# Optimization experiments

Hardware: AMD Instinct MI355X
Metric: run time of the kernel (lower is better)

Reference implementation:

```python
import jax, jax.numpy as jnp
import numpy as np

N0, N1 = 81, 319          # hard-coded split t1[:, :81] / t1[:, 81:]
C_OUT = 64
LAYERS = 5
EPS = 1e-5


def _temporal_conv(X, w1, b1, wc, bc):
    # X: [B, N, T, Cin] -> NCHW with H=N, W=T, kernel (1, 3), VALID
    out_ch = w1.shape[0]
    Xp = jnp.transpose(X, (0, 3, 1, 2))
    dn = ('NCHW', 'OIHW', 'NCHW')
    conv = lambda x, w: jax.lax.conv_general_dilated(x, w, (1, 1), 'VALID', dimension_numbers=dn)
    xc = conv(Xp, wc) + bc[None, :, None, None]
    temp = conv(Xp, w1) + b1[None, :, None, None]
    x_p, x_q = xc[:, :out_ch], xc[:, out_ch:]
    out = (x_p + temp) * jax.nn.sigmoid(x_q)
    return jnp.transpose(out, (0, 2, 3, 1))  # [B, N, T-2, out_ch]


def _het_conv(X0l, X1l, X00, Aaa, Aab, Aba, th1, th2, th3):
    # torch einsum('ij,jklm->kilm', A, X.permute(1,0,2,3)) == einsum('ij,bjtc->bitc', A, X)
    u1 = jnp.einsum('ij,bjtc->bitc', Aaa, X0l)
    u2 = jax.nn.relu(u1 @ th1)
    u3 = jnp.einsum('ij,bjtc->bitc', Aab @ Aba, X0l)
    u4 = jnp.einsum('ij,bjtc->bitc', Aab, X1l)
    u5 = jax.nn.sigmoid(u3 @ th2 + u4 @ th3)
    u6 = jax.nn.relu((u2 + u5) * 0.5)
    return jax.nn.relu(0.9 * u6 + 0.1 * X00)


def setup_inputs() -> dict:
    key = jax.random.key(0)
    ks = jax.random.split(key, 24)
    B, N, T, Cin = 16, 400, 32, 2
    stdv = 1.0 / np.sqrt(C_OUT)
    u = lambda k, shape, s: jax.random.uniform(k, shape, jnp.float32, -s, s)
    inp = {
        'X': jax.random.normal(ks[0], (B, N, T, Cin), jnp.float32),
        'A00': jax.random.uniform(ks[1], (N0, N0), jnp.float32) / N0,
        'A01': jax.random.uniform(ks[2], (N0, N1), jnp.float32) / N1,
        'A10': jax.random.uniform(ks[3], (N1, N0), jnp.float32) / N0,
        'A11': jax.random.uniform(ks[4], (N1, N1), jnp.float32) / N1,
        't1_conv1_w': jax.random.normal(ks[5], (C_OUT, Cin, 1, 3), jnp.float32) * 0.1,
        't1_conv1_b': jnp.zeros((C_OUT,), jnp.float32),
        't1_causal_w': jax.random.normal(ks[6], (2 * C_OUT, Cin, 1, 3), jnp.float32) * 0.1,
        't1_causal_b': jnp.zeros((2 * C_OUT,), jnp.float32),
        'g1_th1': u(ks[7], (LAYERS, C_OUT, C_OUT), stdv),
        'g1_th2': u(ks[8], (LAYERS, C_OUT, C_OUT), stdv),
        'g1_th3': u(ks[9], (LAYERS, C_OUT, C_OUT), stdv),
        'g2_th1': u(ks[10], (LAYERS, C_OUT, C_OUT), stdv),
        'g2_th2': u(ks[11], (LAYERS, C_OUT, C_OUT), stdv),
        'g2_th3': u(ks[12], (LAYERS, C_OUT, C_OUT), stdv),
        'theta': u(ks[13], (C_OUT, C_OUT), stdv),
        't2_conv1_w': jax.random.normal(ks[14], (C_OUT, C_OUT, 1, 3), jnp.float32) * 0.05,
        't2_conv1_b': jnp.zeros((C_OUT,), jnp.float32),
        't2_causal_w': jax.random.normal(ks[15], (2 * C_OUT, C_OUT, 1, 3), jnp.float32) * 0.05,
        't2_causal_b': jnp.zeros((2 * C_OUT,), jnp.float32),
        'bn_gamma': jnp.ones((N,), jnp.float32),
        'bn_beta': jnp.zeros((N,), jnp.float32),
    }
    return inp


def reference(X, A00, A01, A10, A11, t1_conv1_w, t1_conv1_b, t1_causal_w, t1_causal_b,
              g1_th1, g1_th2, g1_th3, g2_th1, g2_th2, g2_th3, theta,
              t2_conv1_w, t2_conv1_b, t2_causal_w, t2_causal_b, bn_gamma, bn_beta):
    t1 = _temporal_conv(X, t1_conv1_w, t1_conv1_b, t1_causal_w, t1_causal_b)  # [B,N,T-2,64]
    X0, X1 = t1[:, :N0], t1[:, N0:]
    u0, u1v = X0, X1
    for i in range(LAYERS):
        u0 = _het_conv(u0, u1v, X0, A00, A01, A10, g1_th1[i], g1_th2[i], g1_th3[i])
        u1v = _het_conv(u1v, u0, X1, A11, A10, A01, g2_th1[i], g2_th2[i], g2_th3[i])
    tk = jnp.concatenate([u0, u1v], axis=1)            # [B,N,T-2,64]
    tk = jax.nn.relu(tk @ theta)
    tk = _temporal_conv(tk, t2_conv1_w, t2_conv1_b, t2_causal_w, t2_causal_b)  # [B,N,T-4,64]
    # BatchNorm2d(num_nodes): channel axis is the node axis (dim 1), training-mode batch stats
    mean = tk.mean(axis=(0, 2, 3), keepdims=True)
    var = tk.var(axis=(0, 2, 3), keepdims=True)
    return (tk - mean) / jnp.sqrt(var + EPS) * bn_gamma[None, :, None, None] + bn_beta[None, :, None, None]
```

## Files before the change

### kernel.cpp

```cpp
#include <hip/hip_runtime.h>


typedef __attribute__((ext_vector_type(8))) short short8v;
typedef __attribute__((ext_vector_type(4))) short short4v;
typedef __attribute__((ext_vector_type(4))) float f32x4;

#define BB 16
#define NA 81
#define NB 319
#define PA 128
#define PB 320
#define M1 1920
#define T1 30
#define T2 28

#define MFMA16 __builtin_amdgcn_mfma_f32_16x16x32_bf16

__device__ __forceinline__ float sigmoidf_(float x){ return 1.0f/(1.0f+__expf(-x)); }
__device__ __forceinline__ short f2bf(float f){
  unsigned u = __float_as_uint(f);
  u += 0x7FFF + ((u>>16)&1);
  return (short)(u>>16);
}
__device__ __forceinline__ float bf2f(short s){
  return __uint_as_float(((unsigned)(unsigned short)s)<<16);
}

__global__ __launch_bounds__(256) void k_prep_mm(const float* __restrict__ A01,
                                                 const float* __restrict__ A10,
                                                 float* __restrict__ Ma) {
  int idx = blockIdx.x*256 + threadIdx.x;
  if (idx >= NA*NA) return;
  int i = idx / NA, j = idx % NA;
  float a = 0.f;
  for (int k = 0; k < NB; ++k) a += A01[i*NB + k]*A10[k*NA + j];
  Ma[idx] = a;
}

__device__ __forceinline__ void packA_one(int f, const float* src, int I, int J,
                                          int ld, int nIt, short* dst) {
  int e = f & 7, l = (f >> 3) & 63, rest = f >> 9;
  int it = rest % nIt, jt = rest / nIt;
  int i = it*16 + (l & 15);
  int j = jt*32 + (l >> 4)*8 + e;
  float v = (i < I && j < J) ? src[i*ld + j] : 0.f;
  dst[f] = f2bf(v);
}

__global__ __launch_bounds__(256) void k_pack_A(
    const float* __restrict__ A00, const float* __restrict__ A01,
    const float* __restrict__ A10, const float* __restrict__ A11,
    const float* __restrict__ Ma,
    short* __restrict__ A00pk, short* __restrict__ Mapk,
    short* __restrict__ A01pk, short* __restrict__ A10pk,
    short* __restrict__ A11pk) {
  int idx = blockIdx.x*256 + threadIdx.x;
  if (idx < 12288)        { packA_one(idx, A00, NA, NA, NA, 8,  A00pk); return; }
  idx -= 12288;
  if (idx < 12288)        { packA_one(idx, Ma,  NA, NA, NA, 8,  Mapk);  return; }
  idx -= 12288;
  if (idx < 40960)        { packA_one(idx, A01, NA, NB, NB, 8,  A01pk); return; }
  idx -= 40960;
  if (idx < 30720)        { packA_one(idx, A10, NB, NA, NA, 20, A10pk); return; }
  idx -= 30720;
  if (idx < 102400)       { packA_one(idx, A11, NB, NB, NB, 20, A11pk); return; }
}

__global__ __launch_bounds__(256) void k_pack_th(
    const float* __restrict__ g1t1, const float* __restrict__ g1t2,
    const float* __restrict__ g1t3, const float* __restrict__ g2t1,
    const float* __restrict__ g2t2, const float* __restrict__ g2t3,
    const float* __restrict__ theta,
    const float* __restrict__ w12, const float* __restrict__ wc2,
    const float* __restrict__ w11, const float* __restrict__ wc1,
    const float* __restrict__ b11, const float* __restrict__ bc1,
    short* __restrict__ thpk, short* __restrict__ thetapk,
    short* __restrict__ W2pk, float* __restrict__ W1t, float* __restrict__ B1t) {
  int idx = blockIdx.x*256 + threadIdx.x;
  if (idx < 122880) {
    int mat = idx / 4096, rem = idx % 4096;
    int ct = rem / 1024, ks = (rem / 512) & 1, l = (rem >> 3) & 63, e = rem & 7;
    int ci = ks*32 + (l >> 4)*8 + e, co = ct*16 + (l & 15);
    int layer = mat / 6, which = mat % 6;
    const float* src = which == 0 ? g1t1 : which == 1 ? g1t2 : which == 2 ? g1t3
                     : which == 3 ? g2t1 : which == 4 ? g2t2 : g2t3;
    thpk[idx] = f2bf(src[layer*4096 + ci*64 + co]);
    return;
  }
  idx -= 122880;
  if (idx < 4096) {
    int ct = idx / 1024, ks = (idx / 512) & 1, l = (idx >> 3) & 63, e = idx & 7;
    int ci = ks*32 + (l >> 4)*8 + e, co = ct*16 + (l & 15);
    thetapk[idx] = f2bf(theta[ci*64 + co]);
    return;
  }
  idx -= 4096;
  if (idx < 36864) {
    int ct = idx / 3072, rem = idx % 3072;
    int ks = rem / 512, l = (rem >> 3) & 63, e = rem & 7;
    int kap = ks*32 + (l >> 4)*8 + e;
    int k = kap >> 6, ci = kap & 63;
    int cc = ct*16 + (l & 15);
    float v = (cc < 64) ? w12[cc*192 + ci*3 + k] : wc2[(cc - 64)*192 + ci*3 + k];
    W2pk[idx] = f2bf(v);
    return;
  }
  idx -= 36864;
  if (idx < 1152) {
    int kk = idx / 192, cc = idx % 192;
    int k = kk >> 1, ci = kk & 1;
    W1t[idx] = (cc < 64) ? w11[cc*6 + ci*3 + k] : wc1[(cc - 64)*6 + ci*3 + k];
    return;
  }
  idx -= 1152;
  if (idx < 192) { B1t[idx] = (idx < 64) ? b11[idx] : bc1[idx - 64]; return; }
}

__global__ __launch_bounds__(192) void k_tconv1(const float* __restrict__ X,
                                                const float* __restrict__ W1t,
                                                const float* __restrict__ B1t,
                                                short* __restrict__ t1a,
                                                short* __restrict__ t1b) {
  __shared__ float xl[64];
  __shared__ float wl[6*192];
  __shared__ float bl[192];
  __shared__ float ol[T1*192];
  int bn = blockIdx.x;
  int b = bn / 400, n = bn % 400;
  int tid = threadIdx.x;
  if (tid < 64) xl[tid] = X[(size_t)bn*64 + tid];
  for (int i2 = tid; i2 < 6*192; i2 += 192) wl[i2] = W1t[i2];
  bl[tid] = B1t[tid];
  __syncthreads();
  float acc[T1];
  float bias = bl[tid];
#pragma unroll
  for (int t = 0; t < T1; ++t) acc[t] = bias;
#pragma unroll
  for (int kk = 0; kk < 6; ++kk) {
    float w = wl[kk*192 + tid];
    int k = kk >> 1, ci = kk & 1;
#pragma unroll
    for (int t = 0; t < T1; ++t) acc[t] += xl[(t + k)*2 + ci]*w;
  }
#pragma unroll
  for (int t = 0; t < T1; ++t) ol[t*192 + tid] = acc[t];
  __syncthreads();
  short* dst = (n < NA) ? (t1a + ((size_t)b*PA + n)*M1)
                        : (t1b + ((size_t)b*PB + (n - NA))*M1);
  for (int p = tid; p < T1*64; p += 192) {
    int t = p >> 6, c = p & 63;
    float v = (ol[t*192 + 64 + c] + ol[t*192 + c])*sigmoidf_(ol[t*192 + 128 + c]);
    dst[p] = f2bf(v);
  }
}

__global__ __launch_bounds__(256) void k_transpose(const short* __restrict__ src,
                                                   short* __restrict__ dst, int Ipad) {
  int lane = threadIdx.x & 63, wv = threadIdx.x >> 6;
  int n = blockIdx.x*64 + lane;
  int b = blockIdx.z;
  const short* sp = src + ((size_t)b*Ipad + n)*M1;
  int mbase = (blockIdx.y*4 + wv)*120;
  for (int k = 0; k < 120; k += 8) {
    int m = mbase + k;
    short8v v = *(const short8v*)(sp + m);
#pragma unroll
    for (int e = 0; e < 8; ++e)
      dst[((size_t)b*M1 + m + e)*Ipad + n] = v[e];
  }
}

template<int KT12, int KT3>
__global__ __launch_bounds__(64, 1) void k_layer_a(
    const short* __restrict__ XT12, int Jp12,
    const short* __restrict__ XT3, int Jp3,
    const short* __restrict__ Apk1, const short* __restrict__ Apk2, int nIt12,
    const short* __restrict__ Apk3, int nIt3,
    const short* __restrict__ th1, const short* __restrict__ th2,
    const short* __restrict__ th3,
    const short* __restrict__ X00, short* __restrict__ uout,
    short* __restrict__ umT, short* __restrict__ g3T,
    int NW, int I, int IpadO) {
  __shared__ short sd[3][32*68];
  int lane = threadIdx.x & 63;
  int ln = lane & 15, qw = lane >> 4;

  int total = NW*30*BB;
  int d = blockIdx.x;
  int logical = (d & 7)*(total >> 3) + (d >> 3);
  int w = logical % NW;
  int rest = logical / NW;
  int mt = rest % 30;
  int b = rest / 30;

  int m0 = mt*64;
  int t = mt;

  short* s1 = sd[0];
  short* s2 = sd[1];
  short* s3 = sd[2];

  short8v x0r[4];
#pragma unroll
  for (int kq = 0; kq < 4; ++kq) {
    int il = kq*8 + (lane >> 3);
    int irow = w*32 + il;
    if (irow >= I) irow = I - 1;
    size_t ro = ((size_t)b*IpadO + irow)*M1 + t*64 + (lane & 7)*8;
    x0r[kq] = *(const short8v*)(X00 + ro);
  }

  {
    f32x4 a3[2][4];
#pragma unroll
    for (int ft = 0; ft < 2; ++ft)
#pragma unroll
      for (int mf = 0; mf < 4; ++mf) a3[ft][mf] = (f32x4)0.f;

    short8v xa[2][4];
    short8v b3f[2][2];
#pragma unroll
    for (int mf = 0; mf < 4; ++mf) {
      size_t ro = ((size_t)b*M1 + m0 + mf*16 + ln)*Jp3 + qw*8;
      xa[0][mf] = *(const short8v*)(XT3 + ro);
    }
    {
      size_t ab = (((size_t)0*nIt3 + w*2)*64 + lane)*8;
      b3f[0][0] = *(const short8v*)(Apk3 + ab);
      b3f[0][1] = *(const short8v*)(Apk3 + ab + 512);
    }
#pragma unroll
    for (int ks = 0; ks < KT3; ++ks) {
      if (ks + 1 < KT3) {
        int nx = (ks + 1) & 1;
#pragma unroll
        for (int mf = 0; mf < 4; ++mf) {
          size_t ro = ((size_t)b*M1 + m0 + mf*16 + ln)*Jp3 + (ks + 1)*32 + qw*8;
          xa[nx][mf] = *(const short8v*)(XT3 + ro);
        }
        size_t ab = (((size_t)(ks + 1)*nIt3 + w*2)*64 + lane)*8;
        b3f[nx][0] = *(const short8v*)(Apk3 + ab);
        b3f[nx][1] = *(const short8v*)(Apk3 + ab + 512);
      }
      int cu = ks & 1;
#pragma unroll
      for (int mf = 0; mf < 4; ++mf) {
        a3[0][mf] = MFMA16(xa[cu][mf], b3f[cu][0], a3[0][mf], 0, 0, 0);
        a3[1][mf] = MFMA16(xa[cu][mf], b3f[cu][1], a3[1][mf], 0, 0, 0);
      }
    }
#pragma unroll
    for (int ft = 0; ft < 2; ++ft)
#pragma unroll
      for (int mf = 0; mf < 4; ++mf) {
        int irow = ft*16 + ln;
        int cc = mf*16 + qw*4;
        short4v v3;
#pragma unroll
        for (int r = 0; r < 4; ++r) v3[r] = f2bf(a3[ft][mf][r]);
        *(short4v*)(s3 + irow*68 + cc) = v3;
      }
  }
  {
    int co = lane;
    size_t cb = ((size_t)b*M1 + t*64 + co)*IpadO + w*32;
#pragma unroll
    for (int kq = 0; kq < 4; ++kq) {
      short8v v;
#pragma unroll
      for (int ii = 0; ii < 8; ++ii) v[ii] = s3[(kq*8 + ii)*68 + co];
      *(short8v*)(g3T + cb + kq*8) = v;
    }
  }

  {
    f32x4 a1[2][4], a2[2][4];
#pragma unroll
    for (int ft = 0; ft < 2; ++ft)
#pragma unroll
      for (int mf = 0; mf < 4; ++mf) { a1[ft][mf] = (f32x4)0.f; a2[ft][mf] = (f32x4)0.f; }

    short8v xa[2][4];
    short8v b1f[2][2], b2f[2][2];
#pragma unroll
    for (int mf = 0; mf < 4; ++mf) {
      size_t ro = ((size_t)b*M1 + m0 + mf*16 + ln)*Jp12 + qw*8;
      xa[0][mf] = *(const short8v*)(XT12 + ro);
    }
    {
      size_t ab = (((size_t)0*nIt12 + w*2)*64 + lane)*8;
      b1f[0][0] = *(const short8v*)(Apk1 + ab);
      b1f[0][1] = *(const short8v*)(Apk1 + ab + 512);
      b2f[0][0] = *(const short8v*)(Apk2 + ab);
      b2f[0][1] = *(const short8v*)(Apk2 + ab + 512);
    }
#pragma unroll
    for (int ks = 0; ks < KT12; ++ks) {
      if (ks + 1 < KT12) {
        int nx = (ks + 1) & 1;
#pragma unroll
        for (int mf = 0; mf < 4; ++mf) {
          size_t ro = ((size_t)b*M1 + m0 + mf*16 + ln)*Jp12 + (ks + 1)*32 + qw*8;
          xa[nx][mf] = *(const short8v*)(XT12 + ro);
        }
        size_t ab = (((size_t)(ks + 1)*nIt12 + w*2)*64 + lane)*8;
        b1f[nx][0] = *(const short8v*)(Apk1 + ab);
        b1f[nx][1] = *(const short8v*)(Apk1 + ab + 512);
        b2f[nx][0] = *(const short8v*)(Apk2 + ab);
        b2f[nx][1] = *(const short8v*)(Apk2 + ab + 512);
      }
      int cu = ks & 1;
#pragma unroll
      for (int mf = 0; mf < 4; ++mf) {
        a1[0][mf] = MFMA16(xa[cu][mf], b1f[cu][0], a1[0][mf], 0, 0, 0);
        a1[1][mf] = MFMA16(xa[cu][mf], b1f[cu][1], a1[1][mf], 0, 0, 0);
        a2[0][mf] = MFMA16(xa[cu][mf], b2f[cu][0], a2[0][mf], 0, 0, 0);
        a2[1][mf] = MFMA16(xa[cu][mf], b2f[cu][1], a2[1][mf], 0, 0, 0);
      }
    }
#pragma unroll
    for (int ft = 0; ft < 2; ++ft)
#pragma unroll
      for (int mf = 0; mf < 4; ++mf) {
        int irow = ft*16 + ln;
        int cc = mf*16 + qw*4;
        short4v v1, v2;
#pragma unroll
        for (int r = 0; r < 4; ++r) {
          v1[r] = f2bf(a1[ft][mf][r]);
          v2[r] = f2bf(a2[ft][mf][r]);
        }
        *(short4v*)(s1 + irow*68 + cc) = v1;
        *(short4v*)(s2 + irow*68 + cc) = v2;
      }
  }

  f32x4 u2a[2][4], u5a[2][4];
#pragma unroll
  for (int fi = 0; fi < 2; ++fi)
#pragma unroll
    for (int ct = 0; ct < 4; ++ct) { u2a[fi][ct] = (f32x4)0.f; u5a[fi][ct] = (f32x4)0.f; }

#pragma unroll
  for (int ks = 0; ks < 2; ++ks) {
    short8v f1[2], f2[2], f3[2];
#pragma unroll
    for (int fi = 0; fi < 2; ++fi) {
      int irow = fi*16 + ln;
      f1[fi] = *(const short8v*)(s1 + irow*68 + ks*32 + qw*8);
      f2[fi] = *(const short8v*)(s2 + irow*68 + ks*32 + qw*8);
      f3[fi] = *(const short8v*)(s3 + irow*68 + ks*32 + qw*8);
    }
#pragma unroll
    for (int ct = 0; ct < 4; ++ct) {
      short8v b1 = *(const short8v*)(th1 + ((ct*2 + ks)*64 + lane)*8);
      short8v b2 = *(const short8v*)(th2 + ((ct*2 + ks)*64 + lane)*8);
      short8v b3 = *(const short8v*)(th3 + ((ct*2 + ks)*64 + lane)*8);
#pragma unroll
      for (int fi = 0; fi < 2; ++fi) {
        u2a[fi][ct] = MFMA16(f1[fi], b1, u2a[fi][ct], 0, 0, 0);
        u5a[fi][ct] = MFMA16(f2[fi], b2, u5a[fi][ct], 0, 0, 0);
        u5a[fi][ct] = MFMA16(f3[fi], b3, u5a[fi][ct], 0, 0, 0);
      }
    }
  }

#pragma unroll
  for (int kq = 0; kq < 4; ++kq) {
    int il = kq*8 + (lane >> 3);
    *(short8v*)(s3 + il*68 + (lane & 7)*8) = x0r[kq];
  }

  short* sg = s1;
#pragma unroll
  for (int fi = 0; fi < 2; ++fi)
#pragma unroll
    for (int ct = 0; ct < 4; ++ct) {
      int co = ct*16 + ln;
#pragma unroll
      for (int r = 0; r < 4; ++r) {
        int il = fi*16 + qw*4 + r;
        int i = w*32 + il;
        short g = 0;
        if (i < I) {
          float u2 = fmaxf(u2a[fi][ct][r], 0.f);
          float u5 = sigmoidf_(u5a[fi][ct][r]);
          float u6 = fmaxf(0.5f*(u2 + u5), 0.f);
          float x0 = bf2f(s3[il*68 + co]);
          g = f2bf(fmaxf(0.9f*u6 + 0.1f*x0, 0.f));
        }
        sg[il*68 + co] = g;
      }
    }

#pragma unroll
  for (int kq = 0; kq < 4; ++kq) {
    int il = kq*8 + (lane >> 3);
    int irow = w*32 + il;
    short8v v = *(const short8v*)(sg + il*68 + (lane & 7)*8);
    if (irow < I)
      *(short8v*)(uout + ((size_t)b*IpadO + irow)*M1 + t*64 + (lane & 7)*8) = v;
  }

  {
    int co = lane;
    size_t cb = ((size_t)b*M1 + t*64 + co)*IpadO + w*32;
#pragma unroll
    for (int kq = 0; kq < 4; ++kq) {
      short8v v;
#pragma unroll
      for (int ii = 0; ii < 8; ++ii) v[ii] = sg[(kq*8 + ii)*68 + co];
      *(short8v*)(umT + cb + kq*8) = v;
    }
  }
}

__global__ __launch_bounds__(64, 1) void k_layer_b(
    const short* __restrict__ X2T,
    const short* __restrict__ X3T,
    const short* __restrict__ X1T,
    const short* __restrict__ ApkS,
    const short* __restrict__ Apk1,
    const short* __restrict__ th1, const short* __restrict__ th2,
    const short* __restrict__ th3,
    const short* __restrict__ X00, short* __restrict__ uout,
    short* __restrict__ umT) {
  const int NW = 10, I = NB, IpadO = PB;
  __shared__ short sd[3][32*68];
  int lane = threadIdx.x & 63;
  int ln = lane & 15, qw = lane >> 4;

  int total = NW*30*BB;
  int d = blockIdx.x;
  int logical = (d & 7)*(total >> 3) + (d >> 3);
  int w = logical % NW;
  int rest = logical / NW;
  int mt = rest % 30;
  int b = rest / 30;

  int m0 = mt*64;
  int t = mt;

  short* s1 = sd[0];
  short* s2 = sd[1];
  short* s3 = sd[2];

  short8v x0r[4];
#pragma unroll
  for (int kq = 0; kq < 4; ++kq) {
    int il = kq*8 + (lane >> 3);
    int irow = w*32 + il;
    if (irow >= I) irow = I - 1;
    size_t ro = ((size_t)b*IpadO + irow)*M1 + t*64 + (lane & 7)*8;
    x0r[kq] = *(const short8v*)(X00 + ro);
  }

  {
    f32x4 a2[2][4], a3[2][4];
#pragma unroll
    for (int ft = 0; ft < 2; ++ft)
#pragma unroll
      for (int mf = 0; mf < 4; ++mf) { a2[ft][mf] = (f32x4)0.f; a3[ft][mf] = (f32x4)0.f; }

    short8v x2[2][4], x3[2][4];
    short8v bf[2][2];
#pragma unroll
    for (int mf = 0; mf < 4; ++mf) {
      size_t ro = ((size_t)b*M1 + m0 + mf*16 + ln)*PA + qw*8;
      x2[0][mf] = *(const short8v*)(X2T + ro);
      x3[0][mf] = *(const short8v*)(X3T + ro);
    }
    {
      size_t ab = (((size_t)0*20 + w*2)*64 + lane)*8;
      bf[0][0] = *(const short8v*)(ApkS + ab);
      bf[0][1] = *(const short8v*)(ApkS + ab + 512);
    }
#pragma unroll
    for (int ks = 0; ks < 3; ++ks) {
      if (ks + 1 < 3) {
        int nx = (ks + 1) & 1;
#pragma unroll
        for (int mf = 0; mf < 4; ++mf) {
          size_t ro = ((size_t)b*M1 + m0 + mf*16 + ln)*PA + (ks + 1)*32 + qw*8;
          x2[nx][mf] = *(const short8v*)(X2T + ro);
          x3[nx][mf] = *(const short8v*)(X3T + ro);
        }
        size_t ab = (((size_t)(ks + 1)*20 + w*2)*64 + lane)*8;
        bf[nx][0] = *(const short8v*)(ApkS + ab);
        bf[nx][1] = *(const short8v*)(ApkS + ab + 512);
      }
      int cu = ks & 1;
#pragma unroll
      for (int mf = 0; mf < 4; ++mf) {
        a2[0][mf] = MFMA16(x2[cu][mf], bf[cu][0], a2[0][mf], 0, 0, 0);
        a2[1][mf] = MFMA16(x2[cu][mf], bf[cu][1], a2[1][mf], 0, 0, 0);
        a3[0][mf] = MFMA16(x3[cu][mf], bf[cu][0], a3[0][mf], 0, 0, 0);
        a3[1][mf] = MFMA16(x3[cu][mf], bf[cu][1], a3[1][mf], 0, 0, 0);
      }
    }
#pragma unroll
    for (int ft = 0; ft < 2; ++ft)
#pragma unroll
      for (int mf = 0; mf < 4; ++mf) {
        int irow = ft*16 + ln;
        int cc = mf*16 + qw*4;
        short4v v2, v3;
#pragma unroll
        for (int r = 0; r < 4; ++r) {
          v2[r] = f2bf(a2[ft][mf][r]);
          v3[r] = f2bf(a3[ft][mf][r]);
        }
        *(short4v*)(s2 + irow*68 + cc) = v2;
        *(short4v*)(s3 + irow*68 + cc) = v3;
      }
  }

  {
    f32x4 a1[2][4];
#pragma unroll
    for (int ft = 0; ft < 2; ++ft)
#pragma unroll
      for (int mf = 0; mf < 4; ++mf) a1[ft][mf] = (f32x4)0.f;

    short8v xa[2][4];
    short8v b1f[2][2];
#pragma unroll
    for (int mf = 0; mf < 4; ++mf) {
      size_t ro = ((size_t)b*M1 + m0 + mf*16 + ln)*PB + qw*8;
      xa[0][mf] = *(const short8v*)(X1T + ro);
    }
    {
      size_t ab = (((size_t)0*20 + w*2)*64 + lane)*8;
      b1f[0][0] = *(const short8v*)(Apk1 + ab);
      b1f[0][1] = *(const short8v*)(Apk1 + ab + 512);
    }
#pragma unroll
    for (int ks = 0; ks < 10; ++ks) {
      if (ks + 1 < 10) {
        int nx = (ks + 1) & 1;
#pragma unroll
        for (int mf = 0; mf < 4; ++mf) {
          size_t ro = ((size_t)b*M1 + m0 + mf*16 + ln)*PB + (ks + 1)*32 + qw*8;
          xa[nx][mf] = *(const short8v*)(X1T + ro);
        }
        size_t ab = (((size_t)(ks + 1)*20 + w*2)*64 + lane)*8;
        b1f[nx][0] = *(const short8v*)(Apk1 + ab);
        b1f[nx][1] = *(const short8v*)(Apk1 + ab + 512);
      }
      int cu = ks & 1;
#pragma unroll
      for (int mf = 0; mf < 4; ++mf) {
        a1[0][mf] = MFMA16(xa[cu][mf], b1f[cu][0], a1[0][mf], 0, 0, 0);
        a1[1][mf] = MFMA16(xa[cu][mf], b1f[cu][1], a1[1][mf], 0, 0, 0);
      }
    }
#pragma unroll
    for (int ft = 0; ft < 2; ++ft)
#pragma unroll
      for (int mf = 0; mf < 4; ++mf) {
        int irow = ft*16 + ln;
        int cc = mf*16 + qw*4;
        short4v v1;
#pragma unroll
        for (int r = 0; r < 4; ++r) v1[r] = f2bf(a1[ft][mf][r]);
        *(short4v*)(s1 + irow*68 + cc) = v1;
      }
  }

  f32x4 u2a[2][4], u5a[2][4];
#pragma unroll
  for (int fi = 0; fi < 2; ++fi)
#pragma unroll
    for (int ct = 0; ct < 4; ++ct) { u2a[fi][ct] = (f32x4)0.f; u5a[fi][ct] = (f32x4)0.f; }

#pragma unroll
  for (int ks = 0; ks < 2; ++ks) {
    short8v f1[2], f2[2], f3[2];
#pragma unroll
    for (int fi = 0; fi < 2; ++fi) {
      int irow = fi*16 + ln;
      f1[fi] = *(const short8v*)(s1 + irow*68 + ks*32 + qw*8);
      f2[fi] = *(const short8v*)(s2 + irow*68 + ks*32 + qw*8);
      f3[fi] = *(const short8v*)(s3 + irow*68 + ks*32 + qw*8);
    }
#pragma unroll
    for (int ct = 0; ct < 4; ++ct) {
      short8v b1 = *(const short8v*)(th1 + ((ct*2 + ks)*64 + lane)*8);
      short8v b2 = *(const short8v*)(th2 + ((ct*2 + ks)*64 + lane)*8);
      short8v b3 = *(const short8v*)(th3 + ((ct*2 + ks)*64 + lane)*8);
#pragma unroll
      for (int fi = 0; fi < 2; ++fi) {
        u2a[fi][ct] = MFMA16(f1[fi], b1, u2a[fi][ct], 0, 0, 0);
        u5a[fi][ct] = MFMA16(f2[fi], b2, u5a[fi][ct], 0, 0, 0);
        u5a[fi][ct] = MFMA16(f3[fi], b3, u5a[fi][ct], 0, 0, 0);
      }
    }
  }

#pragma unroll
  for (int kq = 0; kq < 4; ++kq) {
    int il = kq*8 + (lane >> 3);
    *(short8v*)(s3 + il*68 + (lane & 7)*8) = x0r[kq];
  }

  short* sg = s1;
#pragma unroll
  for (int fi = 0; fi < 2; ++fi)
#pragma unroll
    for (int ct = 0; ct < 4; ++ct) {
      int co = ct*16 + ln;
#pragma unroll
      for (int r = 0; r < 4; ++r) {
        int il = fi*16 + qw*4 + r;
        int i = w*32 + il;
        short g = 0;
        if (i < I) {
          float u2 = fmaxf(u2a[fi][ct][r], 0.f);
          float u5 = sigmoidf_(u5a[fi][ct][r]);
          float u6 = fmaxf(0.5f*(u2 + u5), 0.f);
          float x0 = bf2f(s3[il*68 + co]);
          g = f2bf(fmaxf(0.9f*u6 + 0.1f*x0, 0.f));
        }
        sg[il*68 + co] = g;
      }
    }

#pragma unroll
  for (int kq = 0; kq < 4; ++kq) {
    int il = kq*8 + (lane >> 3);
    int irow = w*32 + il;
    short8v v = *(const short8v*)(sg + il*68 + (lane & 7)*8);
    if (irow < I)
      *(short8v*)(uout + ((size_t)b*IpadO + irow)*M1 + t*64 + (lane & 7)*8) = v;
  }

  {
    int co = lane;
    size_t cb = ((size_t)b*M1 + t*64 + co)*IpadO + w*32;
#pragma unroll
    for (int kq = 0; kq < 4; ++kq) {
      short8v v;
#pragma unroll
      for (int ii = 0; ii < 8; ++ii) v[ii] = sg[(kq*8 + ii)*68 + co];
      *(short8v*)(umT + cb + kq*8) = v;
    }
  }
}

__global__ __launch_bounds__(256) void k_thconv2(const short* __restrict__ u0,
                                                 const short* __restrict__ u1,
                                                 const short* __restrict__ thetapk,
                                                 const short* __restrict__ W2pk,
                                                 const float* __restrict__ b12,
                                                 const float* __restrict__ bc2,
                                                 float* __restrict__ out) {
  __shared__ short lds[34*72];
  int tid = threadIdx.x, lane = tid & 63, wv = tid >> 6;
  int ln = lane & 15, qw = lane >> 4;
  int bn = blockIdx.x;
  int b = blockIdx.y;
  const short* u; int i, Ipad;
  if (bn < NA) { u = u0; i = bn; Ipad = PA; }
  else         { u = u1; i = bn - NA; Ipad = PB; }
  for (int z = tid; z < 4*72; z += 256) lds[30*72 + z] = 0;

  f32x4 ac[2];
  ac[0] = (f32x4)0.f; ac[1] = (f32x4)0.f;
  size_t ubase = ((size_t)b*Ipad + i)*M1;
#pragma unroll
  for (int ks = 0; ks < 2; ++ks) {
    short8v bm = *(const short8v*)(thetapk + ((wv*2 + ks)*64 + lane)*8);
#pragma unroll
    for (int tf = 0; tf < 2; ++tf) {
      short8v af = *(const short8v*)(u + ubase + (tf*16 + ln)*64 + ks*32 + qw*8);
      ac[tf] = MFMA16(af, bm, ac[tf], 0, 0, 0);
    }
  }
#pragma unroll
  for (int tf = 0; tf < 2; ++tf)
#pragma unroll
    for (int r = 0; r < 4; ++r) {
      int t = tf*16 + qw*4 + r;
      if (t < T1) lds[t*72 + wv*16 + ln] = f2bf(fmaxf(ac[tf][r], 0.f));
    }
  __syncthreads();

  f32x4 a3[2][3];
#pragma unroll
  for (int tf = 0; tf < 2; ++tf)
#pragma unroll
    for (int s = 0; s < 3; ++s) a3[tf][s] = (f32x4)0.f;
  for (int ks = 0; ks < 6; ++ks) {
    short8v af[2];
#pragma unroll
    for (int tf = 0; tf < 2; ++tf) {
      int m = (tf*16 + ln)*64 + ks*32 + qw*8;
      af[tf] = *(const short8v*)(lds + (m >> 6)*72 + (m & 63));
    }
#pragma unroll
    for (int s = 0; s < 3; ++s) {
      int ct = wv + s*4;
      short8v bm = *(const short8v*)(W2pk + ((ct*6 + ks)*64 + lane)*8);
#pragma unroll
      for (int tf = 0; tf < 2; ++tf)
        a3[tf][s] = MFMA16(af[tf], bm, a3[tf][s], 0, 0, 0);
    }
  }
  int co = wv*16 + ln;
  float btm = b12[co], bp = bc2[co], bq = bc2[64 + co];
#pragma unroll
  for (int tf = 0; tf < 2; ++tf)
#pragma unroll
    for (int r = 0; r < 4; ++r) {
      int t = tf*16 + qw*4 + r;
      if (t >= T2) continue;
      float tm = a3[tf][0][r] + btm;
      float p  = a3[tf][1][r] + bp;
      float q  = a3[tf][2][r] + bq;
      out[((size_t)(b*400 + bn)*T2 + t)*64 + co] = (p + tm)*sigmoidf_(q);
    }
}

__global__ __launch_bounds__(256) void k_bn_stats(const float* __restrict__ y,
                                                  float* __restrict__ stats) {
  int n = blockIdx.x;
  int tid = threadIdx.x;
  float s = 0.f, ss = 0.f;
  for (int b = 0; b < BB; ++b) {
    const float* p = y + ((size_t)(b*400 + n))*(T2*64);
    for (int i2 = tid; i2 < T2*64; i2 += 256) {
      float v = p[i2];
      s += v; ss += v*v;
    }
  }
  __shared__ float rs[4], rss[4];
  for (int off = 32; off > 0; off >>= 1) {
    s += __shfl_down(s, off);
    ss += __shfl_down(ss, off);
  }
  if ((tid & 63) == 0) { rs[tid >> 6] = s; rss[tid >> 6] = ss; }
  __syncthreads();
  if (tid == 0) {
    float S = rs[0] + rs[1] + rs[2] + rs[3];
    float SS = rss[0] + rss[1] + rss[2] + rss[3];
    float mean = S/28672.f;
    float var = SS/28672.f - mean*mean;
    stats[n] = mean;
    stats[400 + n] = rsqrtf(var + 1e-5f);
  }
}

__global__ void k_bn_apply(float* __restrict__ y, const float* __restrict__ stats,
                           const float* __restrict__ gamma, const float* __restrict__ beta) {
  int idx = blockIdx.x*blockDim.x + threadIdx.x;
  const int total = BB*400*T2*64/4;
  for (; idx < total; idx += gridDim.x*blockDim.x) {
    int e = idx*4;
    int n = (e/(T2*64)) % 400;
    float mean = stats[n];
    float g = gamma[n]*stats[400 + n];
    float bt = beta[n];
    float4 v = ((float4*)y)[idx];
    v.x = (v.x - mean)*g + bt;
    v.y = (v.y - mean)*g + bt;
    v.z = (v.z - mean)*g + bt;
    v.w = (v.w - mean)*g + bt;
    ((float4*)y)[idx] = v;
  }
}

extern "C" void kernel_launch(void* const* d_in, const int* in_sizes, int n_in,
                              void* d_out, int out_size, void* d_ws, size_t ws_size,
                              hipStream_t stream) {
  const float* X     = (const float*)d_in[0];
  const float* A00   = (const float*)d_in[1];
  const float* A01   = (const float*)d_in[2];
  const float* A10   = (const float*)d_in[3];
  const float* A11   = (const float*)d_in[4];
  const float* w11   = (const float*)d_in[5];
  const float* b11   = (const float*)d_in[6];
  const float* wc1   = (const float*)d_in[7];
  const float* bc1   = (const float*)d_in[8];
  const float* g1t1  = (const float*)d_in[9];
  const float* g1t2  = (const float*)d_in[10];
  const float* g1t3  = (const float*)d_in[11];
  const float* g2t1  = (const float*)d_in[12];
  const float* g2t2  = (const float*)d_in[13];
  const float* g2t3  = (const float*)d_in[14];
  const float* theta = (const float*)d_in[15];
  const float* w12   = (const float*)d_in[16];
  const float* b12   = (const float*)d_in[17];
  const float* wc2   = (const float*)d_in[18];
  const float* bc2   = (const float*)d_in[19];
  const float* gamma = (const float*)d_in[20];
  const float* beta  = (const float*)d_in[21];

  short* ws = (short*)d_ws;
  size_t o = 0;
  const size_t szA = (size_t)BB*PA*M1;
  const size_t szB = (size_t)BB*PB*M1;
  short* t1a  = ws + o; o += szA;
  short* t1b  = ws + o; o += szB;
  short* u0   = ws + o; o += szA;
  short* u1   = ws + o; o += szB;
  short* uaT0 = ws + o; o += szA;
  short* uaT1 = ws + o; o += szA;
  short* ubT0 = ws + o; o += szB;
  short* ubT1 = ws + o; o += szB;
  short* g3T  = ws + o; o += szA;
  short* A00pk = ws + o; o += 12288;
  short* Mapk  = ws + o; o += 12288;
  short* A01pk = ws + o; o += 40960;
  short* A10pk = ws + o; o += 30720;
  short* A11pk = ws + o; o += 102400;
  short* thpk    = ws + o; o += 122880;
  short* thetapk = ws + o; o += 4096;
  short* W2pk    = ws + o; o += 36864;
  o = (o + 7) & ~(size_t)7;
  float* fws = (float*)(ws + o);
  float* Ma    = fws;
  float* stats = Ma + 6561;
  float* W1t   = stats + 800;
  float* B1t   = W1t + 1152;

  k_prep_mm<<<26, 256, 0, stream>>>(A01, A10, Ma);
  k_pack_A<<<776, 256, 0, stream>>>(A00, A01, A10, A11, Ma,
                                    A00pk, Mapk, A01pk, A10pk, A11pk);
  k_pack_th<<<646, 256, 0, stream>>>(g1t1, g1t2, g1t3, g2t1, g2t2, g2t3, theta,
                                     w12, wc2, w11, wc1, b11, bc1,
                                     thpk, thetapk, W2pk, W1t, B1t);
  k_tconv1<<<BB*400, 192, 0, stream>>>(X, W1t, B1t, t1a, t1b);
  k_transpose<<<dim3(PA/64, 4, BB), 256, 0, stream>>>(t1a, uaT0, PA);
  k_transpose<<<dim3(PB/64, 4, BB), 256, 0, stream>>>(t1b, ubT0, PB);

  short* uaT[2] = {uaT0, uaT1};
  short* ubT[2] = {ubT0, ubT1};
  for (int l = 0; l < 5; ++l) {
    int pin = l & 1, pout = 1 - pin;
    const short* th = thpk + (size_t)(l*6)*4096;
    k_layer_a<3, 10><<<1440, 64, 0, stream>>>(
        uaT[pin], PA, ubT[pin], PB, A00pk, Mapk, 8, A01pk, 8,
        th + 0*4096, th + 1*4096, th + 2*4096, t1a, u0, uaT[pout], g3T,
        3, NA, PA);
    k_layer_b<<<4800, 64, 0, stream>>>(
        g3T, uaT[pout], ubT[pin], A10pk, A11pk,
        th + 3*4096, th + 4*4096, th + 5*4096, t1b, u1, ubT[pout]);
  }

  k_thconv2<<<dim3(400, BB), 256, 0, stream>>>(u0, u1, thetapk, W2pk, b12, bc2,
                                               (float*)d_out);
  k_bn_stats<<<400, 256, 0, stream>>>((float*)d_out, stats);
  k_bn_apply<<<2048, 256, 0, stream>>>((float*)d_out, stats, gamma, beta);
}
```

Before: 534.0 us.

## Share adjacency B-fragments across two waves via LDS in k_layer_b

k_layer_b now runs 128-thread blocks, with two waves each handling an adjacent time tile for the same node-tile. The packed A10/A11 fragments for that node-tile are loaded once cooperatively into LDS and read by both waves, instead of each wave streaming them from global memory. This halves the global traffic for the B operand and the block count. In exchange it adds a block barrier, more LDS per block, and LDS reads inside the MFMA loop that are no longer prefetched a step ahead.

```diff
diff --git a/kernel.cpp b/kernel.cpp
--- a/kernel.cpp
+++ b/kernel.cpp
@@ -416,7 +416,7 @@
   }
 }
 
-__global__ __launch_bounds__(64, 1) void k_layer_b(
+__global__ __launch_bounds__(128, 1) void k_layer_b(
     const short* __restrict__ X2T,
     const short* __restrict__ X3T,
     const short* __restrict__ X1T,
@@ -427,24 +427,35 @@
     const short* __restrict__ X00, short* __restrict__ uout,
     short* __restrict__ umT) {
   const int NW = 10, I = NB, IpadO = PB;
-  __shared__ short sd[3][32*68];
-  int lane = threadIdx.x & 63;
+  __shared__ short ldsB[13*1024];
+  __shared__ short sd[2][3][32*68];
+  int tid = threadIdx.x;
+  int lane = tid & 63, wv = tid >> 6;
   int ln = lane & 15, qw = lane >> 4;
 
-  int total = NW*30*BB;
+  int total = NW*15*BB;
   int d = blockIdx.x;
   int logical = (d & 7)*(total >> 3) + (d >> 3);
   int w = logical % NW;
   int rest = logical / NW;
-  int mt = rest % 30;
-  int b = rest / 30;
-
+  int mt2 = rest % 15;
+  int b = rest / 15;
+
+  int mt = mt2*2 + wv;
   int m0 = mt*64;
   int t = mt;
 
-  short* s1 = sd[0];
-  short* s2 = sd[1];
-  short* s3 = sd[2];
+  short* s1 = sd[wv][0];
+  short* s2 = sd[wv][1];
+  short* s3 = sd[wv][2];
+
+#pragma unroll
+  for (int c = 0; c < 13; ++c) {
+    const short* src = (c < 3)
+        ? (ApkS + ((size_t)(c*20 + w*2)*64)*8)
+        : (Apk1 + ((size_t)((c - 3)*20 + w*2)*64)*8);
+    *(short8v*)(ldsB + c*1024 + tid*8) = *(const short8v*)(src + tid*8);
+  }
 
   short8v x0r[4];
 #pragma unroll
@@ -455,6 +466,7 @@
     size_t ro = ((size_t)b*IpadO + irow)*M1 + t*64 + (lane & 7)*8;
     x0r[kq] = *(const short8v*)(X00 + ro);
   }
+  __syncthreads();
 
   {
     f32x4 a2[2][4], a3[2][4];
@@ -464,17 +476,11 @@
       for (int mf = 0; mf < 4; ++mf) { a2[ft][mf] = (f32x4)0.f; a3[ft][mf] = (f32x4)0.f; }
 
     short8v x2[2][4], x3[2][4];
-    short8v bf[2][2];
 #pragma unroll
     for (int mf = 0; mf < 4; ++mf) {
       size_t ro = ((size_t)b*M1 + m0 + mf*16 + ln)*PA + qw*8;
       x2[0][mf] = *(const short8v*)(X2T + ro);
       x3[0][mf] = *(const short8v*)(X3T + ro);
-    }
-    {
-      size_t ab = (((size_t)0*20 + w*2)*64 + lane)*8;
-      bf[0][0] = *(const short8v*)(ApkS + ab);
-      bf[0][1] = *(const short8v*)(ApkS + ab + 512);
     }
 #pragma unroll
     for (int ks = 0; ks < 3; ++ks) {
@@ -486,17 +492,16 @@
           x2[nx][mf] = *(const short8v*)(X2T + ro);
           x3[nx][mf] = *(const short8v*)(X3T + ro);
         }
-        size_t ab = (((size_t)(ks + 1)*20 + w*2)*64 + lane)*8;
-        bf[nx][0] = *(const short8v*)(ApkS + ab);
-        bf[nx][1] = *(const short8v*)(ApkS + ab + 512);
       }
       int cu = ks & 1;
+      short8v bf0 = *(const short8v*)(ldsB + ks*1024 + lane*8);
+      short8v bf1 = *(const short8v*)(ldsB + ks*1024 + 512 + lane*8);
 #pragma unroll
       for (int mf = 0; mf < 4; ++mf) {
-        a2[0][mf] = MFMA16(x2[cu][mf], bf[cu][0], a2[0][mf], 0, 0, 0);
-        a2[1][mf] = MFMA16(x2[cu][mf], bf[cu][1], a2[1][mf], 0, 0, 0);
-        a3[0][mf] = MFMA16(x3[cu][mf], bf[cu][0], a3[0][mf], 0, 0, 0);
-        a3[1][mf] = MFMA16(x3[cu][mf], bf[cu][1], a3[1][mf], 0, 0, 0);
+        a2[0][mf] = MFMA16(x2[cu][mf], bf0, a2[0][mf], 0, 0, 0);
+        a2[1][mf] = MFMA16(x2[cu][mf], bf1, a2[1][mf], 0, 0, 0);
+        a3[0][mf] = MFMA16(x3[cu][mf], bf0, a3[0][mf], 0, 0, 0);
+        a3[1][mf] = MFMA16(x3[cu][mf], bf1, a3[1][mf], 0, 0, 0);
       }
     }
 #pragma unroll
@@ -524,16 +529,10 @@
       for (int mf = 0; mf < 4; ++mf) a1[ft][mf] = (f32x4)0.f;
 
     short8v xa[2][4];
-    short8v b1f[2][2];
 #pragma unroll
     for (int mf = 0; mf < 4; ++mf) {
       size_t ro = ((size_t)b*M1 + m0 + mf*16 + ln)*PB + qw*8;
       xa[0][mf] = *(const short8v*)(X1T + ro);
-    }
-    {
-      size_t ab = (((size_t)0*20 + w*2)*64 + lane)*8;
-      b1f[0][0] = *(const short8v*)(Apk1 + ab);
-      b1f[0][1] = *(const short8v*)(Apk1 + ab + 512);
     }
 #pragma unroll
     for (int ks = 0; ks < 10; ++ks) {
@@ -544,15 +543,14 @@
           size_t ro = ((size_t)b*M1 + m0 + mf*16 + ln)*PB + (ks + 1)*32 + qw*8;
           xa[nx][mf] = *(const short8v*)(X1T + ro);
         }
-        size_t ab = (((size_t)(ks + 1)*20 + w*2)*64 + lane)*8;
-        b1f[nx][0] = *(const short8v*)(Apk1 + ab);
-        b1f[nx][1] = *(const short8v*)(Apk1 + ab + 512);
       }
       int cu = ks & 1;
+      short8v bf0 = *(const short8v*)(ldsB + (3 + ks)*1024 + lane*8);
+      short8v bf1 = *(const short8v*)(ldsB + (3 + ks)*1024 + 512 + lane*8);
 #pragma unroll
       for (int mf = 0; mf < 4; ++mf) {
-        a1[0][mf] = MFMA16(xa[cu][mf], b1f[cu][0], a1[0][mf], 0, 0, 0);
-        a1[1][mf] = MFMA16(xa[cu][mf], b1f[cu][1], a1[1][mf], 0, 0, 0);
+        a1[0][mf] = MFMA16(xa[cu][mf], bf0, a1[0][mf], 0, 0, 0);
+        a1[1][mf] = MFMA16(xa[cu][mf], bf1, a1[1][mf], 0, 0, 0);
       }
     }
 #pragma unroll
@@ -843,7 +841,7 @@
         uaT[pin], PA, ubT[pin], PB, A00pk, Mapk, 8, A01pk, 8,
         th + 0*4096, th + 1*4096, th + 2*4096, t1a, u0, uaT[pout], g3T,
         3, NA, PA);
-    k_layer_b<<<4800, 64, 0, stream>>>(
+    k_layer_b<<<2400, 128, 0, stream>>>(
         g3T, uaT[pout], ubT[pin], A10pk, A11pk,
         th + 3*4096, th + 4*4096, th + 5*4096, t1b, u1, ubT[pout]);
   }
```

Result: slower. 590.5 us (+10.6%).
